# Kernel tuning notes

Hardware: AMD Instinct MI355X
Metric: run time of the kernel (lower is better)

The kernel has to match this reference:

```python
import jax, jax.numpy as jnp
import numpy as np

N = 16384          # collocation points
WIDTH = 128        # WavePINN width_size
DEPTH = 6          # WavePINN depth -> 5 hidden-to-hidden layers
PWIDTH = 32        # PsiNetwork width_size
PDEPTH = 2         # PsiNetwork depth -> 1 hidden-to-hidden layer
C0 = 1.0           # base_wave_speed


def _lin(k, out_dim, in_dim):
    return jax.random.normal(k, (out_dim, in_dim), jnp.float32) / np.sqrt(in_dim)


def setup_inputs() -> dict:
    key = jax.random.key(0)
    ks = jax.random.split(key, 20)
    inp = {
        "t": jax.random.uniform(ks[0], (N,), jnp.float32),
        "x": jax.random.uniform(ks[1], (N,), jnp.float32),
        "y": jax.random.uniform(ks[2], (N,), jnp.float32),
        "z": jax.random.uniform(ks[3], (N,), jnp.float32),
        # WavePINN (u_model) params: 4 -> 128 -> (128)x5 -> 1
        "uW_in": _lin(ks[4], WIDTH, 4),
        "ub_in": jnp.zeros((WIDTH,), jnp.float32),
        "uW_hid": jax.random.normal(ks[5], (DEPTH - 1, WIDTH, WIDTH), jnp.float32) / np.sqrt(WIDTH),
        "ub_hid": jnp.zeros((DEPTH - 1, WIDTH), jnp.float32),
        "uW_out": _lin(ks[6], 1, WIDTH),
        "ub_out": jnp.zeros((1,), jnp.float32),
        # PsiNetwork params: 4 -> 32 -> 32 -> 1
        "pW_in": _lin(ks[7], PWIDTH, 4),
        "pb_in": jnp.zeros((PWIDTH,), jnp.float32),
        "pW_hid": jax.random.normal(ks[8], (PDEPTH - 1, PWIDTH, PWIDTH), jnp.float32) / np.sqrt(PWIDTH),
        "pb_hid": jnp.zeros((PDEPTH - 1, PWIDTH), jnp.float32),
        "pW_out": _lin(ks[9], 1, PWIDTH),
        "pb_out": jnp.zeros((1,), jnp.float32),
    }
    return inp


def _mlp(pt, W_in, b_in, W_hid, b_hid, W_out, b_out):
    # eqx.nn.MLP with tanh activation, linear final layer; returns scalar
    h = jnp.tanh(W_in @ pt + b_in)
    for i in range(W_hid.shape[0]):  # static, small layer count
        h = jnp.tanh(W_hid[i] @ h + b_hid[i])
    return (W_out @ h + b_out)[0]


def reference(t, x, y, z,
              uW_in, ub_in, uW_hid, ub_hid, uW_out, ub_out,
              pW_in, pb_in, pW_hid, pb_hid, pW_out, pb_out):
    def point_residual(pt):  # pt: [4] = (t, x, y, z)
        u_fn = lambda p: _mlp(p, uW_in, ub_in, uW_hid, ub_hid, uW_out, ub_out)
        psi = _mlp(pt, pW_in, pb_in, pW_hid, pb_hid, pW_out, pb_out)
        c = C0 * (1.0 + psi)  # modulated wave speed
        # diagonal of the 4x4 Hessian: u_tt, u_xx, u_yy, u_zz
        d = jnp.diagonal(jax.hessian(u_fn)(pt))
        lap = d[1] + d[2] + d[3]
        resid = d[0] - c ** 2 * lap
        has_nan = jnp.any(jnp.isnan(jnp.stack([d[0], d[1], d[2], d[3], c])))
        return jnp.where(has_nan, jnp.float32(jnp.nan), resid)

    pts = jnp.stack([t, x, y, z], axis=1)  # [N, 4]
    return jax.vmap(point_residual)(pts).astype(jnp.float32)
```

## Files before the change

kernel.cpp:

```cpp
#include <hip/hip_runtime.h>
#include <math.h>

#define N_PTS 16384
#define WID   128
#define NHID  5
#define PPB   16
#define CH    9
#define COLS  (PPB*CH)
#define KPAD  132
#define NBLK  (N_PTS/PPB)

typedef __attribute__((ext_vector_type(8))) __bf16 bf16x8;
typedef __attribute__((ext_vector_type(4))) float  f32x4;

__device__ __forceinline__ unsigned short f2bf(float x) {
    unsigned int u = __builtin_bit_cast(unsigned int, x);
    u += 0x7FFFu + ((u >> 16) & 1u);
    return (unsigned short)(u >> 16);
}
__device__ __forceinline__ float bf2f(unsigned short h) {
    unsigned int u = ((unsigned int)h) << 16;
    return __builtin_bit_cast(float, u);
}
__device__ __forceinline__ void split_bf(float x, unsigned short& hi, unsigned short& lo) {
    const unsigned int u = __builtin_bit_cast(unsigned int, x);
    hi = (unsigned short)(u >> 16);
    const float rem = x - __builtin_bit_cast(float, u & 0xFFFF0000u);
    lo = (unsigned short)(__builtin_bit_cast(unsigned int, rem) >> 16);
}
__device__ __forceinline__ unsigned int cvtpk(float v0, float v1) {
    unsigned int r;
    asm("v_cvt_pk_bf16_f32 %0, %1, %2" : "=v"(r) : "v"(v0), "v"(v1));
    return r;
}
__device__ __forceinline__ void split_pk4(const float v0, const float v1,
                                          const float v2, const float v3,
                                          uint2& ph, uint2& pl) {
    const unsigned int h01 = cvtpk(v0, v1);
    const unsigned int h23 = cvtpk(v2, v3);
    const float f0 = __builtin_bit_cast(float, h01 << 16);
    const float f1 = __builtin_bit_cast(float, h01 & 0xFFFF0000u);
    const float f2 = __builtin_bit_cast(float, h23 << 16);
    const float f3 = __builtin_bit_cast(float, h23 & 0xFFFF0000u);
    ph = make_uint2(h01, h23);
    pl = make_uint2(cvtpk(v0 - f0, v1 - f1), cvtpk(v2 - f2, v3 - f3));
}
__device__ __forceinline__ void fast_tanh_g(float x, float& a, float& g) {
    x = fminf(fmaxf(x, -40.0f), 40.0f);
    const float e = __builtin_amdgcn_exp2f(2.88539008177793f * x);
    const float r = __builtin_amdgcn_rcpf(e + 1.0f);
    a = 1.0f - 2.0f * r;
    g = 4.0f * e * r * r;
}

__global__ __launch_bounds__(64) void pack_w(const float* __restrict__ uWhid,
                                             unsigned short* __restrict__ whi,
                                             unsigned short* __restrict__ wlo)
{
    const int f  = blockIdx.x;
    const int v  = threadIdx.x;
    const int l  = f >> 5;
    const int s  = (f >> 3) & 3;
    const int rt = f & 7;
    const int row = rt*16 + (v & 15);
    const int k0  = s*32 + ((v >> 4) << 3);
    const float* src = uWhid + (l*WID + row)*WID + k0;
    unsigned short h[8], lo[8];
#pragma unroll
    for (int j = 0; j < 8; ++j) {
        const float x = src[j];
        h[j]  = f2bf(x);
        lo[j] = f2bf(x - bf2f(h[j]));
    }
    const int off = f*512 + v*8;
    *reinterpret_cast<ushort4*>(&whi[off])   = make_ushort4(h[0],h[1],h[2],h[3]);
    *reinterpret_cast<ushort4*>(&whi[off+4]) = make_ushort4(h[4],h[5],h[6],h[7]);
    *reinterpret_cast<ushort4*>(&wlo[off])   = make_ushort4(lo[0],lo[1],lo[2],lo[3]);
    *reinterpret_cast<ushort4*>(&wlo[off+4]) = make_ushort4(lo[4],lo[5],lo[6],lo[7]);
}

__global__ __launch_bounds__(256, 2) void resid_mfma(
    const float* __restrict__ gt, const float* __restrict__ gx,
    const float* __restrict__ gy, const float* __restrict__ gz,
    const float* __restrict__ uWin, const float* __restrict__ ubin,
    const float* __restrict__ ubhid, const float* __restrict__ uWout,
    const unsigned short* __restrict__ whi, const unsigned short* __restrict__ wlo,
    const float* __restrict__ pWin, const float* __restrict__ pbin,
    const float* __restrict__ pWhid, const float* __restrict__ pbhid,
    const float* __restrict__ pWout, const float* __restrict__ pbout,
    float* __restrict__ out)
{
    __shared__ unsigned short act_h[COLS*KPAD];
    __shared__ unsigned short act_l[COLS*KPAD];
    __shared__ float pts4[PPB][4];
    __shared__ float psi_h1[PPB][32];
    __shared__ float c2s[PPB];
    __shared__ float psum[4][PPB][4];

    const int tid  = threadIdx.x;
    const int rq   = tid >> 6;
    const int v    = tid & 63;
    const int base = blockIdx.x * PPB;

    if (tid < PPB) {
        pts4[tid][0] = gt[base+tid]; pts4[tid][1] = gx[base+tid];
        pts4[tid][2] = gy[base+tid]; pts4[tid][3] = gz[base+tid];
    }
    __syncthreads();

    {
        const int p  = tid & 15;
        const int gg = tid >> 4;
        const float q0 = pts4[p][0], q1 = pts4[p][1], q2 = pts4[p][2], q3 = pts4[p][3];
#pragma unroll
        for (int c4 = 0; c4 < 2; ++c4) {
            float vf[CH][4];
#pragma unroll
            for (int i = 0; i < 4; ++i) {
                const int n = gg*8 + c4*4 + i;
                const float4 wr = *reinterpret_cast<const float4*>(&uWin[n*4]);
                const float z = ubin[n] + wr.x*q0 + wr.y*q1 + wr.z*q2 + wr.w*q3;
                float a, g;  fast_tanh_g(z, a, g);
                const float m = -2.0f * a * g;
                vf[0][i] = a;
                vf[1][i] = g*wr.x; vf[2][i] = g*wr.y; vf[3][i] = g*wr.z; vf[4][i] = g*wr.w;
                vf[5][i] = m*wr.x*wr.x; vf[6][i] = m*wr.y*wr.y;
                vf[7][i] = m*wr.z*wr.z; vf[8][i] = m*wr.w*wr.w;
            }
            const int n0 = gg*8 + c4*4;
#pragma unroll
            for (int ch = 0; ch < CH; ++ch) {
                uint2 ph, pl;
                split_pk4(vf[ch][0], vf[ch][1], vf[ch][2], vf[ch][3], ph, pl);
                const int off = (ch*PPB + p)*KPAD + n0;
                *reinterpret_cast<uint2*>(&act_h[off]) = ph;
                *reinterpret_cast<uint2*>(&act_l[off]) = pl;
            }
        }
    }
    {
        const int p = tid >> 4, sub = tid & 15;
        const float q0 = pts4[p][0], q1 = pts4[p][1], q2 = pts4[p][2], q3 = pts4[p][3];
#pragma unroll
        for (int rr = 0; rr < 2; ++rr) {
            const int r = sub*2 + rr;
            const float4 wr = *reinterpret_cast<const float4*>(&pWin[r*4]);
            float a, gd;
            fast_tanh_g(pbin[r] + wr.x*q0 + wr.y*q1 + wr.z*q2 + wr.w*q3, a, gd);
            psi_h1[p][r] = a;
        }
    }
    __syncthreads();

    {
        const int p = tid >> 4, sub = tid & 15;
        float partial = 0.f;
#pragma unroll
        for (int rr = 0; rr < 2; ++rr) {
            const int r = sub*2 + rr;
            float s = pbhid[r];
#pragma unroll
            for (int j = 0; j < 32; ++j) s = fmaf(pWhid[r*32+j], psi_h1[p][j], s);
            float a, gd;  fast_tanh_g(s, a, gd);
            partial = fmaf(pWout[r], a, partial);
        }
        partial += __shfl_xor(partial, 1);
        partial += __shfl_xor(partial, 2);
        partial += __shfl_xor(partial, 4);
        partial += __shfl_xor(partial, 8);
        if (sub == 0) {
            const float c = 1.0f + pbout[0] + partial;
            c2s[p] = c * c;
        }
    }

    f32x4 acc[2][CH];
    const int g4    = (v >> 4) << 2;
    const int lrow0 = rq * 32;
    const int bcol  = v & 15;
    const int krow  = (v >> 4) << 3;

    for (int l = 0; l < NHID; ++l) {
#pragma unroll
        for (int rt = 0; rt < 2; ++rt) {
            acc[rt][0] = *reinterpret_cast<const f32x4*>(&ubhid[l*WID + lrow0 + rt*16 + g4]);
#pragma unroll
            for (int ct = 1; ct < CH; ++ct) acc[rt][ct] = (f32x4){0.f,0.f,0.f,0.f};
        }
#pragma unroll
        for (int s = 0; s < 4; ++s) {
            bf16x8 bh[CH], bl[CH], ah[2], al[2];
            const int kof = s*32 + krow;
            const int fb  = ((l*4 + s)*8 + rq*2)*512 + v*8;
#pragma unroll
            for (int rt = 0; rt < 2; ++rt) {
                ah[rt] = *reinterpret_cast<const bf16x8*>(&whi[fb + rt*512]);
                al[rt] = *reinterpret_cast<const bf16x8*>(&wlo[fb + rt*512]);
            }
#pragma unroll
            for (int ct = 0; ct < CH; ++ct) {
                const int off = (ct*PPB + bcol)*KPAD + kof;
                bh[ct] = *reinterpret_cast<const bf16x8*>(&act_h[off]);
                bl[ct] = *reinterpret_cast<const bf16x8*>(&act_l[off]);
            }
            __builtin_amdgcn_s_setprio(1);
#pragma unroll
            for (int rt = 0; rt < 2; ++rt)
#pragma unroll
                for (int ct = 0; ct < CH; ++ct)
                    acc[rt][ct] = __builtin_amdgcn_mfma_f32_16x16x32_bf16(ah[rt], bh[ct], acc[rt][ct], 0,0,0);
#pragma unroll
            for (int rt = 0; rt < 2; ++rt)
#pragma unroll
                for (int ct = 0; ct < CH; ++ct)
                    acc[rt][ct] = __builtin_amdgcn_mfma_f32_16x16x32_bf16(ah[rt], bl[ct], acc[rt][ct], 0,0,0);
#pragma unroll
            for (int rt = 0; rt < 2; ++rt)
#pragma unroll
                for (int ct = 0; ct < CH; ++ct)
                    acc[rt][ct] = __builtin_amdgcn_mfma_f32_16x16x32_bf16(al[rt], bh[ct], acc[rt][ct], 0,0,0);
            __builtin_amdgcn_s_setprio(0);
        }

        if (l < NHID-1) {
            const int p = v & 15;
            uint2 ph[2][CH], pl[2][CH];
#pragma unroll
            for (int rt = 0; rt < 2; ++rt) {
                float vf[CH][4];
#pragma unroll
                for (int r = 0; r < 4; ++r) {
                    float a, g;  fast_tanh_g(acc[rt][0][r], a, g);
                    const float m2a = -2.0f * a;
                    vf[0][r] = a;
#pragma unroll
                    for (int d = 0; d < 4; ++d) {
                        const float zd  = acc[rt][1+d][r];
                        const float zdd = acc[rt][5+d][r];
                        vf[1+d][r] = g * zd;
                        vf[5+d][r] = g * fmaf(m2a*zd, zd, zdd);
                    }
                }
#pragma unroll
                for (int ch = 0; ch < CH; ++ch)
                    split_pk4(vf[ch][0], vf[ch][1], vf[ch][2], vf[ch][3], ph[rt][ch], pl[rt][ch]);
            }
            __syncthreads();
#pragma unroll
            for (int rt = 0; rt < 2; ++rt) {
                const int n0 = lrow0 + rt*16 + g4;
#pragma unroll
                for (int ch = 0; ch < CH; ++ch) {
                    const int off = (ch*PPB + p)*KPAD + n0;
                    *reinterpret_cast<uint2*>(&act_h[off]) = ph[rt][ch];
                    *reinterpret_cast<uint2*>(&act_l[off]) = pl[rt][ch];
                }
            }
            __syncthreads();
        }
    }

    float part0 = 0.f, part1 = 0.f, part2 = 0.f, part3 = 0.f;
#pragma unroll
    for (int rt = 0; rt < 2; ++rt) {
        const float4 w4 = *reinterpret_cast<const float4*>(&uWout[lrow0 + rt*16 + g4]);
#pragma unroll
        for (int r = 0; r < 4; ++r) {
            const float wr = (&w4.x)[r];
            float a, g;  fast_tanh_g(acc[rt][0][r], a, g);
            const float zd0 = acc[rt][1][r], zd1 = acc[rt][2][r];
            const float zd2 = acc[rt][3][r], zd3 = acc[rt][4][r];
            part0 = fmaf(wr, g*(acc[rt][5][r] - 2.0f*a*zd0*zd0), part0);
            part1 = fmaf(wr, g*(acc[rt][6][r] - 2.0f*a*zd1*zd1), part1);
            part2 = fmaf(wr, g*(acc[rt][7][r] - 2.0f*a*zd2*zd2), part2);
            part3 = fmaf(wr, g*(acc[rt][8][r] - 2.0f*a*zd3*zd3), part3);
        }
    }
    part0 += __shfl_xor(part0, 16); part0 += __shfl_xor(part0, 32);
    part1 += __shfl_xor(part1, 16); part1 += __shfl_xor(part1, 32);
    part2 += __shfl_xor(part2, 16); part2 += __shfl_xor(part2, 32);
    part3 += __shfl_xor(part3, 16); part3 += __shfl_xor(part3, 32);
    if (v < PPB) {
        psum[rq][v][0] = part0; psum[rq][v][1] = part1;
        psum[rq][v][2] = part2; psum[rq][v][3] = part3;
    }
    __syncthreads();
    if (tid < PPB) {
        const float d0  = psum[0][tid][0] + psum[1][tid][0] + psum[2][tid][0] + psum[3][tid][0];
        const float lap = (psum[0][tid][1] + psum[1][tid][1] + psum[2][tid][1] + psum[3][tid][1])
                        + (psum[0][tid][2] + psum[1][tid][2] + psum[2][tid][2] + psum[3][tid][2])
                        + (psum[0][tid][3] + psum[1][tid][3] + psum[2][tid][3] + psum[3][tid][3]);
        out[base+tid] = d0 - c2s[tid]*lap;
    }
}

__global__ __launch_bounds__(64) void psi_kernel(
    const float* __restrict__ gt, const float* __restrict__ gx,
    const float* __restrict__ gy, const float* __restrict__ gz,
    const float* __restrict__ pWin, const float* __restrict__ pbin,
    const float* __restrict__ pWhid, const float* __restrict__ pbhid,
    const float* __restrict__ pWout, const float* __restrict__ pbout,
    float* __restrict__ c2)
{
    const int i = blockIdx.x * 64 + threadIdx.x;
    if (i >= N_PTS) return;
    const float q0 = gt[i], q1 = gx[i], q2 = gy[i], q3 = gz[i];
    float h1[32];
#pragma unroll
    for (int r = 0; r < 32; ++r) {
        float s = pbin[r] + pWin[r*4+0]*q0 + pWin[r*4+1]*q1
                + pWin[r*4+2]*q2 + pWin[r*4+3]*q3;
        h1[r] = tanhf(s);
    }
    float psi = pbout[0];
#pragma unroll 4
    for (int r = 0; r < 32; ++r) {
        float s = pbhid[r];
#pragma unroll
        for (int j = 0; j < 32; ++j) s = fmaf(pWhid[r*32+j], h1[j], s);
        psi = fmaf(pWout[r], tanhf(s), psi);
    }
    const float c = 1.0f + psi;
    c2[i] = c * c;
}

__global__ __launch_bounds__(256, 2) void resid_f32(
    const float* __restrict__ gt, const float* __restrict__ gx,
    const float* __restrict__ gy, const float* __restrict__ gz,
    const float* __restrict__ uWin, const float* __restrict__ ubin,
    const float* __restrict__ uWhid, const float* __restrict__ ubhid,
    const float* __restrict__ uWout,
    const float* __restrict__ c2g, float* __restrict__ out)
{
    __shared__ float act[WID][16*CH];
    __shared__ float ptsh[16][4];
    __shared__ float dsh[16][4];
    const int tid  = threadIdx.x;
    const int rg   = tid >> 4;
    const int p    = tid & 15;
    const int base = blockIdx.x * 16;
    const int row0 = rg * 8;
    const int c0   = p * CH;
    if (tid < 16) {
        ptsh[tid][0] = gt[base+tid]; ptsh[tid][1] = gx[base+tid];
        ptsh[tid][2] = gy[base+tid]; ptsh[tid][3] = gz[base+tid];
    }
    __syncthreads();
    {
        const float q0 = ptsh[p][0], q1 = ptsh[p][1], q2 = ptsh[p][2], q3 = ptsh[p][3];
#pragma unroll
        for (int r = 0; r < 8; ++r) {
            const int row = row0 + r;
            const float w0 = uWin[row*4+0], w1 = uWin[row*4+1];
            const float w2 = uWin[row*4+2], w3 = uWin[row*4+3];
            const float zz = ubin[row] + w0*q0 + w1*q1 + w2*q2 + w3*q3;
            const float a  = tanhf(zz);
            const float g  = 1.0f - a*a;
            const float m2 = -2.0f * a * g;
            act[row][c0+0] = a;
            act[row][c0+1] = g*w0; act[row][c0+2] = g*w1;
            act[row][c0+3] = g*w2; act[row][c0+4] = g*w3;
            act[row][c0+5] = m2*w0*w0; act[row][c0+6] = m2*w1*w1;
            act[row][c0+7] = m2*w2*w2; act[row][c0+8] = m2*w3*w3;
        }
    }
    __syncthreads();
    for (int l = 0; l < NHID; ++l) {
        const float* __restrict__ Wl = uWhid + l*WID*WID;
        float accv[8][CH];
#pragma unroll
        for (int r = 0; r < 8; ++r) {
            accv[r][0] = ubhid[l*WID + row0 + r];
#pragma unroll
            for (int c = 1; c < CH; ++c) accv[r][c] = 0.0f;
        }
        for (int k0 = 0; k0 < WID; k0 += 4) {
            float4 wv[8];
#pragma unroll
            for (int r = 0; r < 8; ++r)
                wv[r] = *reinterpret_cast<const float4*>(&Wl[(row0+r)*WID + k0]);
            float hv[4][CH];
#pragma unroll
            for (int kk = 0; kk < 4; ++kk)
#pragma unroll
                for (int c = 0; c < CH; ++c) hv[kk][c] = act[k0+kk][c0+c];
#pragma unroll
            for (int kk = 0; kk < 4; ++kk)
#pragma unroll
                for (int r = 0; r < 8; ++r) {
                    const float wk = reinterpret_cast<const float*>(&wv[r])[kk];
#pragma unroll
                    for (int c = 0; c < CH; ++c) accv[r][c] = fmaf(wk, hv[kk][c], accv[r][c]);
                }
        }
        __syncthreads();
#pragma unroll
        for (int r = 0; r < 8; ++r) {
            const int row = row0 + r;
            const float a = tanhf(accv[r][0]);
            const float g = 1.0f - a*a;
            act[row][c0+0] = a;
#pragma unroll
            for (int i = 0; i < 4; ++i) {
                const float zd  = accv[r][1+i];
                const float zdd = accv[r][5+i];
                act[row][c0+1+i] = g*zd;
                act[row][c0+5+i] = g*(zdd - 2.0f*a*zd*zd);
            }
        }
        __syncthreads();
    }
    if (tid < 64) {
        const int pp = tid >> 2, ii = tid & 3;
        float s = 0.0f;
        for (int k = 0; k < WID; ++k) s = fmaf(uWout[k], act[k][pp*CH+5+ii], s);
        dsh[pp][ii] = s;
    }
    __syncthreads();
    if (tid < 16) {
        const float d0  = dsh[tid][0];
        const float lap = dsh[tid][1] + dsh[tid][2] + dsh[tid][3];
        out[base+tid] = d0 - c2g[base+tid]*lap;
    }
}

extern "C" void kernel_launch(void* const* d_in, const int* in_sizes, int n_in,
                              void* d_out, int out_size, void* d_ws, size_t ws_size,
                              hipStream_t stream)
{
    const float* gt    = (const float*)d_in[0];
    const float* gx    = (const float*)d_in[1];
    const float* gy    = (const float*)d_in[2];
    const float* gz    = (const float*)d_in[3];
    const float* uWin  = (const float*)d_in[4];
    const float* ubin  = (const float*)d_in[5];
    const float* uWhid = (const float*)d_in[6];
    const float* ubhid = (const float*)d_in[7];
    const float* uWout = (const float*)d_in[8];
    const float* pWin  = (const float*)d_in[10];
    const float* pbin  = (const float*)d_in[11];
    const float* pWhid = (const float*)d_in[12];
    const float* pbhid = (const float*)d_in[13];
    const float* pWout = (const float*)d_in[14];
    const float* pbout = (const float*)d_in[15];
    float* out = (float*)d_out;

    if (ws_size >= 327680) {
        unsigned short* whi = (unsigned short*)d_ws;
        unsigned short* wlo = whi + 81920;
        pack_w<<<160, 64, 0, stream>>>(uWhid, whi, wlo);
        resid_mfma<<<NBLK, 256, 0, stream>>>(gt, gx, gy, gz,
                uWin, ubin, ubhid, uWout, whi, wlo,
                pWin, pbin, pWhid, pbhid, pWout, pbout, out);
    } else {
        float* c2 = (float*)d_ws;
        psi_kernel<<<N_PTS/64, 64, 0, stream>>>(gt, gx, gy, gz,
                pWin, pbin, pWhid, pbhid, pWout, pbout, c2);
        resid_f32<<<N_PTS/16, 256, 0, stream>>>(gt, gx, gy, gz,
                uWin, ubin, uWhid, ubhid, uWout, c2, out);
    }
}
```

Before: 77.30 us.

## Merge spatial second-derivative channels into single Laplacian channel

Propagates the sum of the x, y, z second-derivative tangents as one channel instead of three. The sum is valid because the second-order recurrence is linear in the incoming second derivative, with the squared first-derivative terms summed together. This cuts the MFMA column tiles, LDS activation storage and elementwise work from nine channels to seven. It slightly changes floating-point rounding order.

```diff
diff --git a/kernel.cpp b/kernel.cpp
--- a/kernel.cpp
+++ b/kernel.cpp
@@ -5,8 +5,8 @@
 #define WID   128
 #define NHID  5
 #define PPB   16
-#define CH    9
-#define COLS  (PPB*CH)
+#define NCH   7
+#define COLS  (PPB*NCH)
 #define KPAD  132
 #define NBLK  (N_PTS/PPB)
 
@@ -95,7 +95,7 @@
     __shared__ float pts4[PPB][4];
     __shared__ float psi_h1[PPB][32];
     __shared__ float c2s[PPB];
-    __shared__ float psum[4][PPB][4];
+    __shared__ float psum[4][PPB][2];
 
     const int tid  = threadIdx.x;
     const int rq   = tid >> 6;
@@ -114,7 +114,7 @@
         const float q0 = pts4[p][0], q1 = pts4[p][1], q2 = pts4[p][2], q3 = pts4[p][3];
 #pragma unroll
         for (int c4 = 0; c4 < 2; ++c4) {
-            float vf[CH][4];
+            float vf[NCH][4];
 #pragma unroll
             for (int i = 0; i < 4; ++i) {
                 const int n = gg*8 + c4*4 + i;
@@ -124,12 +124,12 @@
                 const float m = -2.0f * a * g;
                 vf[0][i] = a;
                 vf[1][i] = g*wr.x; vf[2][i] = g*wr.y; vf[3][i] = g*wr.z; vf[4][i] = g*wr.w;
-                vf[5][i] = m*wr.x*wr.x; vf[6][i] = m*wr.y*wr.y;
-                vf[7][i] = m*wr.z*wr.z; vf[8][i] = m*wr.w*wr.w;
+                vf[5][i] = m*wr.x*wr.x;
+                vf[6][i] = m*(wr.y*wr.y + wr.z*wr.z + wr.w*wr.w);
             }
             const int n0 = gg*8 + c4*4;
 #pragma unroll
-            for (int ch = 0; ch < CH; ++ch) {
+            for (int ch = 0; ch < NCH; ++ch) {
                 uint2 ph, pl;
                 split_pk4(vf[ch][0], vf[ch][1], vf[ch][2], vf[ch][3], ph, pl);
                 const int off = (ch*PPB + p)*KPAD + n0;
@@ -174,7 +174,7 @@
         }
     }
 
-    f32x4 acc[2][CH];
+    f32x4 acc[2][NCH];
     const int g4    = (v >> 4) << 2;
     const int lrow0 = rq * 32;
     const int bcol  = v & 15;
@@ -185,11 +185,11 @@
         for (int rt = 0; rt < 2; ++rt) {
             acc[rt][0] = *reinterpret_cast<const f32x4*>(&ubhid[l*WID + lrow0 + rt*16 + g4]);
 #pragma unroll
-            for (int ct = 1; ct < CH; ++ct) acc[rt][ct] = (f32x4){0.f,0.f,0.f,0.f};
+            for (int ct = 1; ct < NCH; ++ct) acc[rt][ct] = (f32x4){0.f,0.f,0.f,0.f};
         }
 #pragma unroll
         for (int s = 0; s < 4; ++s) {
-            bf16x8 bh[CH], bl[CH], ah[2], al[2];
+            bf16x8 bh[NCH], bl[NCH], ah[2], al[2];
             const int kof = s*32 + krow;
             const int fb  = ((l*4 + s)*8 + rq*2)*512 + v*8;
 #pragma unroll
@@ -198,7 +198,7 @@
                 al[rt] = *reinterpret_cast<const bf16x8*>(&wlo[fb + rt*512]);
             }
 #pragma unroll
-            for (int ct = 0; ct < CH; ++ct) {
+            for (int ct = 0; ct < NCH; ++ct) {
                 const int off = (ct*PPB + bcol)*KPAD + kof;
                 bh[ct] = *reinterpret_cast<const bf16x8*>(&act_h[off]);
                 bl[ct] = *reinterpret_cast<const bf16x8*>(&act_l[off]);
@@ -207,42 +207,42 @@
 #pragma unroll
             for (int rt = 0; rt < 2; ++rt)
 #pragma unroll
-                for (int ct = 0; ct < CH; ++ct)
+                for (int ct = 0; ct < NCH; ++ct)
                     acc[rt][ct] = __builtin_amdgcn_mfma_f32_16x16x32_bf16(ah[rt], bh[ct], acc[rt][ct], 0,0,0);
 #pragma unroll
             for (int rt = 0; rt < 2; ++rt)
 #pragma unroll
-                for (int ct = 0; ct < CH; ++ct)
+                for (int ct = 0; ct < NCH; ++ct)
                     acc[rt][ct] = __builtin_amdgcn_mfma_f32_16x16x32_bf16(ah[rt], bl[ct], acc[rt][ct], 0,0,0);
 #pragma unroll
             for (int rt = 0; rt < 2; ++rt)
 #pragma unroll
-                for (int ct = 0; ct < CH; ++ct)
+                for (int ct = 0; ct < NCH; ++ct)
                     acc[rt][ct] = __builtin_amdgcn_mfma_f32_16x16x32_bf16(al[rt], bh[ct], acc[rt][ct], 0,0,0);
             __builtin_amdgcn_s_setprio(0);
         }
 
         if (l < NHID-1) {
             const int p = v & 15;
-            uint2 ph[2][CH], pl[2][CH];
+            uint2 ph[2][NCH], pl[2][NCH];
 #pragma unroll
             for (int rt = 0; rt < 2; ++rt) {
-                float vf[CH][4];
+                float vf[NCH][4];
 #pragma unroll
                 for (int r = 0; r < 4; ++r) {
                     float a, g;  fast_tanh_g(acc[rt][0][r], a, g);
                     const float m2a = -2.0f * a;
+                    const float zt = acc[rt][1][r], zx = acc[rt][2][r];
+                    const float zy = acc[rt][3][r], zz = acc[rt][4][r];
                     vf[0][r] = a;
-#pragma unroll
-                    for (int d = 0; d < 4; ++d) {
-                        const float zd  = acc[rt][1+d][r];
-                        const float zdd = acc[rt][5+d][r];
-                        vf[1+d][r] = g * zd;
-                        vf[5+d][r] = g * fmaf(m2a*zd, zd, zdd);
-                    }
+                    vf[1][r] = g * zt;  vf[2][r] = g * zx;
+                    vf[3][r] = g * zy;  vf[4][r] = g * zz;
+                    vf[5][r] = g * fmaf(m2a*zt, zt, acc[rt][5][r]);
+                    const float s2 = fmaf(zx, zx, fmaf(zy, zy, zz*zz));
+                    vf[6][r] = g * fmaf(m2a, s2, acc[rt][6][r]);
                 }
 #pragma unroll
-                for (int ch = 0; ch < CH; ++ch)
+                for (int ch = 0; ch < NCH; ++ch)
                     split_pk4(vf[ch][0], vf[ch][1], vf[ch][2], vf[ch][3], ph[rt][ch], pl[rt][ch]);
             }
             __syncthreads();
@@ -250,7 +250,7 @@
             for (int rt = 0; rt < 2; ++rt) {
                 const int n0 = lrow0 + rt*16 + g4;
 #pragma unroll
-                for (int ch = 0; ch < CH; ++ch) {
+                for (int ch = 0; ch < NCH; ++ch) {
                     const int off = (ch*PPB + p)*KPAD + n0;
                     *reinterpret_cast<uint2*>(&act_h[off]) = ph[rt][ch];
                     *reinterpret_cast<uint2*>(&act_l[off]) = pl[rt][ch];
@@ -260,7 +260,7 @@
         }
     }
 
-    float part0 = 0.f, part1 = 0.f, part2 = 0.f, part3 = 0.f;
+    float part0 = 0.f, part1 = 0.f;
 #pragma unroll
     for (int rt = 0; rt < 2; ++rt) {
         const float4 w4 = *reinterpret_cast<const float4*>(&uWout[lrow0 + rt*16 + g4]);
@@ -268,28 +268,23 @@
         for (int r = 0; r < 4; ++r) {
             const float wr = (&w4.x)[r];
             float a, g;  fast_tanh_g(acc[rt][0][r], a, g);
-            const float zd0 = acc[rt][1][r], zd1 = acc[rt][2][r];
-            const float zd2 = acc[rt][3][r], zd3 = acc[rt][4][r];
-            part0 = fmaf(wr, g*(acc[rt][5][r] - 2.0f*a*zd0*zd0), part0);
-            part1 = fmaf(wr, g*(acc[rt][6][r] - 2.0f*a*zd1*zd1), part1);
-            part2 = fmaf(wr, g*(acc[rt][7][r] - 2.0f*a*zd2*zd2), part2);
-            part3 = fmaf(wr, g*(acc[rt][8][r] - 2.0f*a*zd3*zd3), part3);
+            const float m2a = -2.0f * a;
+            const float zt = acc[rt][1][r], zx = acc[rt][2][r];
+            const float zy = acc[rt][3][r], zz = acc[rt][4][r];
+            part0 = fmaf(wr, g * fmaf(m2a*zt, zt, acc[rt][5][r]), part0);
+            const float s2 = fmaf(zx, zx, fmaf(zy, zy, zz*zz));
+            part1 = fmaf(wr, g * fmaf(m2a, s2, acc[rt][6][r]), part1);
         }
     }
     part0 += __shfl_xor(part0, 16); part0 += __shfl_xor(part0, 32);
     part1 += __shfl_xor(part1, 16); part1 += __shfl_xor(part1, 32);
-    part2 += __shfl_xor(part2, 16); part2 += __shfl_xor(part2, 32);
-    part3 += __shfl_xor(part3, 16); part3 += __shfl_xor(part3, 32);
     if (v < PPB) {
         psum[rq][v][0] = part0; psum[rq][v][1] = part1;
-        psum[rq][v][2] = part2; psum[rq][v][3] = part3;
     }
     __syncthreads();
     if (tid < PPB) {
         const float d0  = psum[0][tid][0] + psum[1][tid][0] + psum[2][tid][0] + psum[3][tid][0];
-        const float lap = (psum[0][tid][1] + psum[1][tid][1] + psum[2][tid][1] + psum[3][tid][1])
-                        + (psum[0][tid][2] + psum[1][tid][2] + psum[2][tid][2] + psum[3][tid][2])
-                        + (psum[0][tid][3] + psum[1][tid][3] + psum[2][tid][3] + psum[3][tid][3]);
+        const float lap = psum[0][tid][1] + psum[1][tid][1] + psum[2][tid][1] + psum[3][tid][1];
         out[base+tid] = d0 - c2s[tid]*lap;
     }
 }
@@ -332,7 +327,7 @@
     const float* __restrict__ uWout,
     const float* __restrict__ c2g, float* __restrict__ out)
 {
-    __shared__ float act[WID][16*CH];
+    __shared__ float act[WID][16*9];
     __shared__ float ptsh[16][4];
     __shared__ float dsh[16][4];
     const int tid  = threadIdx.x;
@@ -340,7 +335,7 @@
     const int p    = tid & 15;
     const int base = blockIdx.x * 16;
     const int row0 = rg * 8;
-    const int c0   = p * CH;
+    const int c0   = p * 9;
     if (tid < 16) {
         ptsh[tid][0] = gt[base+tid]; ptsh[tid][1] = gx[base+tid];
         ptsh[tid][2] = gy[base+tid]; ptsh[tid][3] = gz[base+tid];
@@ -367,30 +362,30 @@
     __syncthreads();
     for (int l = 0; l < NHID; ++l) {
         const float* __restrict__ Wl = uWhid + l*WID*WID;
-        float accv[8][CH];
+        float accv[8][9];
 #pragma unroll
         for (int r = 0; r < 8; ++r) {
             accv[r][0] = ubhid[l*WID + row0 + r];
 #pragma unroll
-            for (int c = 1; c < CH; ++c) accv[r][c] = 0.0f;
+            for (int c = 1; c < 9; ++c) accv[r][c] = 0.0f;
         }
         for (int k0 = 0; k0 < WID; k0 += 4) {
             float4 wv[8];
 #pragma unroll
             for (int r = 0; r < 8; ++r)
                 wv[r] = *reinterpret_cast<const float4*>(&Wl[(row0+r)*WID + k0]);
-            float hv[4][CH];
+            float hv[4][9];
 #pragma unroll
             for (int kk = 0; kk < 4; ++kk)
 #pragma unroll
-                for (int c = 0; c < CH; ++c) hv[kk][c] = act[k0+kk][c0+c];
+                for (int c = 0; c < 9; ++c) hv[kk][c] = act[k0+kk][c0+c];
 #pragma unroll
             for (int kk = 0; kk < 4; ++kk)
 #pragma unroll
                 for (int r = 0; r < 8; ++r) {
                     const float wk = reinterpret_cast<const float*>(&wv[r])[kk];
 #pragma unroll
-                    for (int c = 0; c < CH; ++c) accv[r][c] = fmaf(wk, hv[kk][c], accv[r][c]);
+                    for (int c = 0; c < 9; ++c) accv[r][c] = fmaf(wk, hv[kk][c], accv[r][c]);
                 }
         }
         __syncthreads();
@@ -413,7 +408,7 @@
     if (tid < 64) {
         const int pp = tid >> 2, ii = tid & 3;
         float s = 0.0f;
-        for (int k = 0; k < WID; ++k) s = fmaf(uWout[k], act[k][pp*CH+5+ii], s);
+        for (int k = 0; k < WID; ++k) s = fmaf(uWout[k], act[k][pp*9+5+ii], s);
         dsh[pp][ii] = s;
     }
     __syncthreads();
```

After: 64.66 us. 1.2x faster.
